# Kernel tuning notes

Hardware: AMD Instinct MI355X
Metric: run time of the kernel (lower is better)

## Reference

```python
import jax, jax.numpy as jnp
import numpy as np

TEMP = 0.05


def setup_inputs() -> dict:
    key = jax.random.key(0)
    k1, k2, k3 = jax.random.split(key, 3)
    B, D, NC = 1024, 256, 50000  # batch, feat dim, num clusters
    inputs = jax.random.normal(k1, (B, D), dtype=jnp.float32)
    targets = jax.random.randint(k2, (B,), 0, NC, dtype=jnp.int64)
    feats = jax.random.normal(k3, (2 * NC, D), dtype=jnp.float32)
    # memory bank rows are kept L2-normalized by the module's update rule
    feats = feats / jnp.linalg.norm(feats, axis=1, keepdims=True)
    return {"inputs": inputs, "targets": targets, "features": feats}


def reference(inputs, targets, features):
    # F.normalize(inputs, dim=1)
    x = inputs / jnp.linalg.norm(inputs, axis=1, keepdims=True)
    # outputs = x @ features.T / temp  -> [B, 2*NC]
    logits = jnp.matmul(x, features.T) / TEMP
    mean_logits, hard_logits = jnp.split(logits, 2, axis=1)  # each [B, NC]

    def ce(lg):
        logp = jax.nn.log_softmax(lg, axis=1)
        return -jnp.take_along_axis(logp, targets[:, None], axis=1).mean()

    loss = 0.5 * (ce(hard_logits) + ce(mean_logits))
    return loss
```

## Files before the change

kernel.cpp:

```cpp
#include <hip/hip_runtime.h>
#include <math.h>

#define BATCH 1024
#define DIM   256
#define NCL   50000
#define TOTC  100000
#define NSLICE 16

typedef __attribute__((ext_vector_type(8)))  short bf16x8;
typedef __attribute__((ext_vector_type(16))) float f32x16;

__device__ __forceinline__ unsigned int f2bf(float f) {
    unsigned int u = __float_as_uint(f);
    return (u + 0x7FFFu + ((u >> 16) & 1u)) >> 16;
}

__global__ __launch_bounds__(64) void k_prep(const float* __restrict__ in,
                                             const int* __restrict__ tgt,
                                             const float* __restrict__ feats,
                                             unsigned short* __restrict__ xnT,
                                             float* __restrict__ Sx,
                                             float* __restrict__ z) {
    const int b = blockIdx.x;
    const int t = threadIdx.x;
    float4 v = *(const float4*)&in[b * DIM + t * 4];
    float ss = v.x * v.x + v.y * v.y + v.z * v.z + v.w * v.w;
#pragma unroll
    for (int o = 1; o < 64; o <<= 1) ss += __shfl_xor(ss, o, 64);
    const float sc = 1.0f / sqrtf(ss);
    float4 w;
    w.x = v.x * sc; w.y = v.y * sc; w.z = v.z * sc; w.w = v.w * sc;

    uint2 p;
    p.x = f2bf(w.x) | (f2bf(w.y) << 16);
    p.y = f2bf(w.z) | (f2bf(w.w) << 16);
    *(uint2*)((char*)xnT + (t >> 1) * 16384 + b * 16 + (t & 1) * 8) = p;

    const int tb = tgt[b];
#pragma unroll
    for (int h = 0; h < 2; ++h) {
        const int row = tb + h * NCL;
        float4 f = *(const float4*)&feats[row * DIM + t * 4];
        float d = w.x * f.x + w.y * f.y + w.z * f.z + w.w * f.w;
#pragma unroll
        for (int o = 1; o < 64; o <<= 1) d += __shfl_xor(d, o, 64);
        if (t == 0) z[b * 2 + h] = d * 20.0f;
    }
    if (t < 32) Sx[b * 32 + t] = 0.0f;
}

__global__ __launch_bounds__(256, 3) void k_main(const unsigned short* __restrict__ xnT,
                                                 const float* __restrict__ feats,
                                                 float* __restrict__ Sx) {
    __shared__ unsigned short Ab[64 * 256];

    const int tid  = threadIdx.x;
    const int lane = tid & 63;
    const int wn   = tid >> 6;
    const int l31  = lane & 31;
    const int hi   = lane >> 5;
    const int cb0  = blockIdx.x * 64;
    float* Ss = Sx + (blockIdx.x & (NSLICE - 1)) * (BATCH * 2);

#pragma unroll
    for (int it = 0; it < 8; ++it) {
        const int idx = it * 256 + tid;
        const int r = idx >> 5;
        const int c = idx & 31;
        int gr = cb0 + r;
        if (gr > TOTC - 1) gr = TOTC - 1;
        const float4 f0 = *(const float4*)&feats[(size_t)gr * DIM + c * 8];
        const float4 f1 = *(const float4*)&feats[(size_t)gr * DIM + c * 8 + 4];
        uint4 pk;
        pk.x = f2bf(f0.x) | (f2bf(f0.y) << 16);
        pk.y = f2bf(f0.z) | (f2bf(f0.w) << 16);
        pk.z = f2bf(f1.x) | (f2bf(f1.y) << 16);
        pk.w = f2bf(f1.z) | (f2bf(f1.w) << 16);
        *(uint4*)((char*)Ab + c * 1024 + ((r * 16) ^ ((c & 7) << 4))) = pk;
    }
    __syncthreads();

    const bool mixed = (cb0 < NCL && cb0 + 63 >= NCL) || (cb0 + 63 >= TOTC);
    const int  halfsel = (cb0 >= NCL) ? 1 : 0;

    float sr0[4][2], sr1[4][2];

#pragma unroll
    for (int p = 0; p < 4; ++p) {
        const unsigned short* bb0 = xnT + (size_t)hi * 8192
                                  + (size_t)(p * 256 + wn * 64 + l31) * 8;
        const unsigned short* bb1 = bb0 + 256;

        f32x16 acc[2][2];
#pragma unroll
        for (int mt = 0; mt < 2; ++mt) {
            acc[mt][0] = (f32x16)(0.0f);
            acc[mt][1] = (f32x16)(0.0f);
        }

#pragma unroll 4
        for (int kk = 0; kk < 16; ++kk) {
            const bf16x8 b0 = *(const bf16x8*)(bb0 + (size_t)kk * 16384);
            const bf16x8 b1 = *(const bf16x8*)(bb1 + (size_t)kk * 16384);
            const int ch = kk * 2 + hi;
            const int kbase = ch * 1024;
            const int key = (ch & 7) << 4;
#pragma unroll
            for (int mt = 0; mt < 2; ++mt) {
                const bf16x8 a = *(const bf16x8*)((const char*)Ab + kbase
                                   + ((mt * 512 + l31 * 16) ^ key));
                acc[mt][0] = __builtin_amdgcn_mfma_f32_32x32x16_bf16(a, b0, acc[mt][0], 0, 0, 0);
                acc[mt][1] = __builtin_amdgcn_mfma_f32_32x32x16_bf16(a, b1, acc[mt][1], 0, 0, 0);
            }
        }

        if (!mixed) {
#pragma unroll
            for (int nn = 0; nn < 2; ++nn) {
                float s = 0.0f;
#pragma unroll
                for (int mt = 0; mt < 2; ++mt)
#pragma unroll
                    for (int r = 0; r < 16; ++r)
                        s += __expf(fmaf(acc[mt][nn][r], 20.0f, -20.0f));
                s += __shfl_xor(s, 32, 64);
                sr0[p][nn] = s;
                sr1[p][nn] = 0.0f;
            }
        } else {
#pragma unroll
            for (int nn = 0; nn < 2; ++nn) {
                float sh0 = 0.0f, sh1 = 0.0f;
#pragma unroll
                for (int mt = 0; mt < 2; ++mt)
#pragma unroll
                    for (int r = 0; r < 16; ++r) {
                        const int cl = cb0 + mt * 32 +
                                       (r & 3) + 8 * (r >> 2) + 4 * hi;
                        const bool valid = cl < TOTC;
                        float e = __expf(fmaf(acc[mt][nn][r], 20.0f, -20.0f));
                        e = valid ? e : 0.0f;
                        sh0 += (cl < NCL) ? e : 0.0f;
                        sh1 += (cl < NCL) ? 0.0f : e;
                    }
                sh0 += __shfl_xor(sh0, 32, 64);
                sh1 += __shfl_xor(sh1, 32, 64);
                sr0[p][nn] = sh0;
                sr1[p][nn] = sh1;
            }
        }
    }

    if (hi == 0) {
#pragma unroll
        for (int p = 0; p < 4; ++p)
#pragma unroll
            for (int nn = 0; nn < 2; ++nn) {
                const int col = p * 256 + wn * 64 + nn * 32 + l31;
                if (!mixed) {
                    atomicAdd(&Ss[col * 2 + halfsel], sr0[p][nn]);
                } else {
                    atomicAdd(&Ss[col * 2 + 0], sr0[p][nn]);
                    atomicAdd(&Ss[col * 2 + 1], sr1[p][nn]);
                }
            }
    }
}

__global__ __launch_bounds__(256) void k_loss(const float* __restrict__ Sx,
                                              const float* __restrict__ z,
                                              float* __restrict__ out) {
    const int t = threadIdx.x;
    float part = 0.0f;
    for (int r = t; r < BATCH; r += 256) {
        float s0 = 0.0f, s1 = 0.0f;
#pragma unroll
        for (int sl = 0; sl < NSLICE; ++sl) {
            s0 += Sx[sl * (BATCH * 2) + r * 2 + 0];
            s1 += Sx[sl * (BATCH * 2) + r * 2 + 1];
        }
        part += 40.0f + logf(s0) + logf(s1) - z[r * 2 + 0] - z[r * 2 + 1];
    }
#pragma unroll
    for (int o = 1; o < 64; o <<= 1) part += __shfl_xor(part, o, 64);
    __shared__ float ws[4];
    if ((t & 63) == 0) ws[t >> 6] = part;
    __syncthreads();
    if (t == 0) {
        const float tot = ws[0] + ws[1] + ws[2] + ws[3];
        out[0] = 0.5f * tot / (float)BATCH;
    }
}

extern "C" void kernel_launch(void* const* d_in, const int* in_sizes, int n_in,
                              void* d_out, int out_size, void* d_ws, size_t ws_size,
                              hipStream_t stream) {
    const float* inputs  = (const float*)d_in[0];
    const int*   targets = (const int*)d_in[1];
    const float* feats   = (const float*)d_in[2];
    float* out = (float*)d_out;

    unsigned short* xnT = (unsigned short*)d_ws;
    float* Sx = (float*)(xnT + BATCH * DIM);
    float* zt = Sx + NSLICE * BATCH * 2;

    k_prep<<<BATCH, 64, 0, stream>>>(inputs, targets, feats, xnT, Sx, zt);
    const int nblk = (TOTC + 63) / 64;
    k_main<<<nblk, 256, 0, stream>>>(xnT, feats, Sx);
    k_loss<<<1, 256, 0, stream>>>(Sx, zt, out);
}
```

Baseline: 93.38 us.

## Split main kernel into pure and boundary-tile kernels with exp2 and setprio

Splits the main GEMM+softmax-sum kernel into a specialized kernel for tiles that fall entirely within one half and a small kernel for the two boundary tiles. The pure kernel drops the mixed-tile branching and the second partial-sum array, and raises launch bounds to 4 blocks per CU. It also uses exp2f with a prescaled constant and sets wave priority around the MFMA loop. The goal is lower register pressure and higher occupancy, at the cost of one extra kernel launch.

```diff
diff --git a/kernel.cpp b/kernel.cpp
--- a/kernel.cpp
+++ b/kernel.cpp
@@ -6,6 +6,7 @@
 #define NCL   50000
 #define TOTC  100000
 #define NSLICE 16
+#define K2E   28.853900817779268f
 
 typedef __attribute__((ext_vector_type(8)))  short bf16x8;
 typedef __attribute__((ext_vector_type(16))) float f32x16;
@@ -49,7 +50,27 @@
     if (t < 32) Sx[b * 32 + t] = 0.0f;
 }
 
-__global__ __launch_bounds__(256, 3) void k_main(const unsigned short* __restrict__ xnT,
+__device__ __forceinline__ void stage_A(unsigned short* Ab,
+                                        const float* __restrict__ feats,
+                                        int cb0, int tid) {
+#pragma unroll
+    for (int it = 0; it < 8; ++it) {
+        const int idx = it * 256 + tid;
+        const int r = idx >> 5;
+        const int c = idx & 31;
+        const int gr = cb0 + r;
+        const float4 f0 = *(const float4*)&feats[(size_t)gr * DIM + c * 8];
+        const float4 f1 = *(const float4*)&feats[(size_t)gr * DIM + c * 8 + 4];
+        uint4 pk;
+        pk.x = f2bf(f0.x) | (f2bf(f0.y) << 16);
+        pk.y = f2bf(f0.z) | (f2bf(f0.w) << 16);
+        pk.z = f2bf(f1.x) | (f2bf(f1.y) << 16);
+        pk.w = f2bf(f1.z) | (f2bf(f1.w) << 16);
+        *(uint4*)((char*)Ab + c * 1024 + ((r * 16) ^ ((c & 7) << 4))) = pk;
+    }
+}
+
+__global__ __launch_bounds__(256, 4) void k_pure(const unsigned short* __restrict__ xnT,
                                                  const float* __restrict__ feats,
                                                  float* __restrict__ Sx) {
     __shared__ unsigned short Ab[64 * 256];
@@ -59,8 +80,80 @@
     const int wn   = tid >> 6;
     const int l31  = lane & 31;
     const int hi   = lane >> 5;
-    const int cb0  = blockIdx.x * 64;
-    float* Ss = Sx + (blockIdx.x & (NSLICE - 1)) * (BATCH * 2);
+    const int g    = (blockIdx.x < 781) ? blockIdx.x : blockIdx.x + 1;
+    const int cb0  = g * 64;
+    const int halfsel = (cb0 >= NCL) ? 1 : 0;
+    float* Ss = Sx + (g & (NSLICE - 1)) * (BATCH * 2);
+
+    stage_A(Ab, feats, cb0, tid);
+    __syncthreads();
+
+    float sr[4][2];
+
+#pragma unroll
+    for (int p = 0; p < 4; ++p) {
+        const unsigned short* bb0 = xnT + (size_t)hi * 8192
+                                  + (size_t)(p * 256 + wn * 64 + l31) * 8;
+        const unsigned short* bb1 = bb0 + 256;
+
+        f32x16 acc00 = (f32x16)(0.0f), acc01 = (f32x16)(0.0f);
+        f32x16 acc10 = (f32x16)(0.0f), acc11 = (f32x16)(0.0f);
+
+        __builtin_amdgcn_s_setprio(1);
+#pragma unroll 4
+        for (int kk = 0; kk < 16; ++kk) {
+            const bf16x8 b0 = *(const bf16x8*)(bb0 + (size_t)kk * 16384);
+            const bf16x8 b1 = *(const bf16x8*)(bb1 + (size_t)kk * 16384);
+            const int ch = kk * 2 + hi;
+            const int kbase = ch * 1024;
+            const int key = (ch & 7) << 4;
+            const bf16x8 a0 = *(const bf16x8*)((const char*)Ab + kbase + ((l31 * 16) ^ key));
+            const bf16x8 a1 = *(const bf16x8*)((const char*)Ab + kbase + ((512 + l31 * 16) ^ key));
+            acc00 = __builtin_amdgcn_mfma_f32_32x32x16_bf16(a0, b0, acc00, 0, 0, 0);
+            acc01 = __builtin_amdgcn_mfma_f32_32x32x16_bf16(a0, b1, acc01, 0, 0, 0);
+            acc10 = __builtin_amdgcn_mfma_f32_32x32x16_bf16(a1, b0, acc10, 0, 0, 0);
+            acc11 = __builtin_amdgcn_mfma_f32_32x32x16_bf16(a1, b1, acc11, 0, 0, 0);
+        }
+        __builtin_amdgcn_s_setprio(0);
+
+        float s0 = 0.0f, s1 = 0.0f;
+#pragma unroll
+        for (int r = 0; r < 16; ++r) {
+            s0 += exp2f(fmaf(acc00[r], K2E, -K2E));
+            s0 += exp2f(fmaf(acc10[r], K2E, -K2E));
+            s1 += exp2f(fmaf(acc01[r], K2E, -K2E));
+            s1 += exp2f(fmaf(acc11[r], K2E, -K2E));
+        }
+        s0 += __shfl_xor(s0, 32, 64);
+        s1 += __shfl_xor(s1, 32, 64);
+        sr[p][0] = s0;
+        sr[p][1] = s1;
+    }
+
+    if (hi == 0) {
+#pragma unroll
+        for (int p = 0; p < 4; ++p)
+#pragma unroll
+            for (int nn = 0; nn < 2; ++nn) {
+                const int col = p * 256 + wn * 64 + nn * 32 + l31;
+                atomicAdd(&Ss[col * 2 + halfsel], sr[p][nn]);
+            }
+    }
+}
+
+__global__ __launch_bounds__(256) void k_mixed(const unsigned short* __restrict__ xnT,
+                                               const float* __restrict__ feats,
+                                               float* __restrict__ Sx) {
+    __shared__ unsigned short Ab[64 * 256];
+
+    const int tid  = threadIdx.x;
+    const int lane = tid & 63;
+    const int wn   = tid >> 6;
+    const int l31  = lane & 31;
+    const int hi   = lane >> 5;
+    const int g    = (blockIdx.x == 0) ? 781 : 1562;
+    const int cb0  = g * 64;
+    float* Ss = Sx + (g & (NSLICE - 1)) * (BATCH * 2);
 
 #pragma unroll
     for (int it = 0; it < 8; ++it) {
@@ -80,11 +173,6 @@
     }
     __syncthreads();
 
-    const bool mixed = (cb0 < NCL && cb0 + 63 >= NCL) || (cb0 + 63 >= TOTC);
-    const int  halfsel = (cb0 >= NCL) ? 1 : 0;
-
-    float sr0[4][2], sr1[4][2];
-
 #pragma unroll
     for (int p = 0; p < 4; ++p) {
         const unsigned short* bb0 = xnT + (size_t)hi * 8192
@@ -93,10 +181,7 @@
 
         f32x16 acc[2][2];
 #pragma unroll
-        for (int mt = 0; mt < 2; ++mt) {
-            acc[mt][0] = (f32x16)(0.0f);
-            acc[mt][1] = (f32x16)(0.0f);
-        }
+        for (int mt = 0; mt < 2; ++mt) { acc[mt][0] = (f32x16)(0.0f); acc[mt][1] = (f32x16)(0.0f); }
 
 #pragma unroll 4
         for (int kk = 0; kk < 16; ++kk) {
@@ -114,56 +199,28 @@
             }
         }
 
-        if (!mixed) {
-#pragma unroll
-            for (int nn = 0; nn < 2; ++nn) {
-                float s = 0.0f;
-#pragma unroll
-                for (int mt = 0; mt < 2; ++mt)
-#pragma unroll
-                    for (int r = 0; r < 16; ++r)
-                        s += __expf(fmaf(acc[mt][nn][r], 20.0f, -20.0f));
-                s += __shfl_xor(s, 32, 64);
-                sr0[p][nn] = s;
-                sr1[p][nn] = 0.0f;
+#pragma unroll
+        for (int nn = 0; nn < 2; ++nn) {
+            float sh0 = 0.0f, sh1 = 0.0f;
+#pragma unroll
+            for (int mt = 0; mt < 2; ++mt)
+#pragma unroll
+                for (int r = 0; r < 16; ++r) {
+                    const int cl = cb0 + mt * 32 + (r & 3) + 8 * (r >> 2) + 4 * hi;
+                    const bool valid = cl < TOTC;
+                    float e = exp2f(fmaf(acc[mt][nn][r], K2E, -K2E));
+                    e = valid ? e : 0.0f;
+                    sh0 += (cl < NCL) ? e : 0.0f;
+                    sh1 += (cl < NCL) ? 0.0f : e;
+                }
+            sh0 += __shfl_xor(sh0, 32, 64);
+            sh1 += __shfl_xor(sh1, 32, 64);
+            if (hi == 0) {
+                const int col = p * 256 + wn * 64 + nn * 32 + l31;
+                atomicAdd(&Ss[col * 2 + 0], sh0);
+                atomicAdd(&Ss[col * 2 + 1], sh1);
             }
-        } else {
-#pragma unroll
-            for (int nn = 0; nn < 2; ++nn) {
-                float sh0 = 0.0f, sh1 = 0.0f;
-#pragma unroll
-                for (int mt = 0; mt < 2; ++mt)
-#pragma unroll
-                    for (int r = 0; r < 16; ++r) {
-                        const int cl = cb0 + mt * 32 +
-                                       (r & 3) + 8 * (r >> 2) + 4 * hi;
-                        const bool valid = cl < TOTC;
-                        float e = __expf(fmaf(acc[mt][nn][r], 20.0f, -20.0f));
-                        e = valid ? e : 0.0f;
-                        sh0 += (cl < NCL) ? e : 0.0f;
-                        sh1 += (cl < NCL) ? 0.0f : e;
-                    }
-                sh0 += __shfl_xor(sh0, 32, 64);
-                sh1 += __shfl_xor(sh1, 32, 64);
-                sr0[p][nn] = sh0;
-                sr1[p][nn] = sh1;
-            }
-        }
-    }
-
-    if (hi == 0) {
-#pragma unroll
-        for (int p = 0; p < 4; ++p)
-#pragma unroll
-            for (int nn = 0; nn < 2; ++nn) {
-                const int col = p * 256 + wn * 64 + nn * 32 + l31;
-                if (!mixed) {
-                    atomicAdd(&Ss[col * 2 + halfsel], sr0[p][nn]);
-                } else {
-                    atomicAdd(&Ss[col * 2 + 0], sr0[p][nn]);
-                    atomicAdd(&Ss[col * 2 + 1], sr1[p][nn]);
-                }
-            }
+        }
     }
 }
 
@@ -205,7 +262,7 @@
     float* zt = Sx + NSLICE * BATCH * 2;
 
     k_prep<<<BATCH, 64, 0, stream>>>(inputs, targets, feats, xnT, Sx, zt);
-    const int nblk = (TOTC + 63) / 64;
-    k_main<<<nblk, 256, 0, stream>>>(xnT, feats, Sx);
+    k_pure<<<1561, 256, 0, stream>>>(xnT, feats, Sx);
+    k_mixed<<<2, 256, 0, stream>>>(xnT, feats, Sx);
     k_loss<<<1, 256, 0, stream>>>(Sx, zt, out);
 }
```

New measurement: 105.3 us. 12.7% more time.
